# Kernel tuning notes

Hardware: AMD Instinct MI355X
Metric: run time of the kernel (lower is better)

The kernel has to match this reference:

```python
import jax, jax.numpy as jnp
import numpy as np

NEG_INF = -9e15


def setup_inputs() -> dict:
    key = jax.random.key(0)
    k1, k2, k3, k4, k5, k6 = jax.random.split(key, 6)
    B, N, F_IN, F_OUT = 16, 2048, 256, 128
    inputs = jax.random.normal(k1, (B, N, F_IN), dtype=jnp.float32)
    adj_matrix = jax.random.randint(k2, (B, N, N), 0, 2, dtype=jnp.int32)
    W = jax.random.normal(k3, (F_OUT, F_IN), dtype=jnp.float32) * (1.0 / np.sqrt(F_IN))
    b_W = jax.random.normal(k4, (F_OUT,), dtype=jnp.float32) * 0.02
    a = jax.random.normal(k5, (1, 2 * F_OUT), dtype=jnp.float32) * (1.0 / np.sqrt(2 * F_OUT))
    b_a = jax.random.normal(k6, (1,), dtype=jnp.float32) * 0.02
    return {"inputs": inputs, "adj_matrix": adj_matrix, "W": W, "b_W": b_W, "a": a, "b_a": b_a}


def reference(inputs, adj_matrix, W, b_W, a, b_a):
    # wh: [B, N, H]
    wh = jnp.einsum('bnf,hf->bnh', inputs, W) + b_W
    H = wh.shape[-1]
    # linear_self_W([wh_i, wh_j]) = a1.wh_i + a2.wh_j + b  (rank-1 linear over concat)
    a1 = a[0, :H]
    a2 = a[0, H:]
    src = jnp.einsum('bnh,h->bn', wh, a1)  # [B, N] contribution of row node i
    dst = jnp.einsum('bnh,h->bn', wh, a2)  # [B, N] contribution of col node j
    e = jax.nn.leaky_relu(src[:, :, None] + dst[:, None, :] + b_a[0], negative_slope=0.01)
    e = jnp.where(adj_matrix > 0, e, NEG_INF)
    att = jax.nn.softmax(e, axis=-1)  # dropout in eval mode = identity
    return jax.nn.elu(jnp.einsum('bij,bjh->bih', att, wh))
```

## Files before the change

kernel.cpp:

```cpp
#include <hip/hip_runtime.h>


#define BDIM 16
#define NDIM 2048
#define FIN 256
#define HDIM 128
#define LOG2E 1.4426950408889634f

typedef short short8 __attribute__((ext_vector_type(8)));
typedef float floatx4 __attribute__((ext_vector_type(4)));
typedef int intx4 __attribute__((ext_vector_type(4)));

__device__ __forceinline__ unsigned short f2bf(float x) {
    unsigned int u = __float_as_uint(x);
    unsigned int r = (u + 0x7fffu + ((u >> 16) & 1u)) >> 16;
    return (unsigned short)r;
}
__device__ __forceinline__ float bf2f(unsigned short s) {
    return __uint_as_float(((unsigned int)s) << 16);
}
__device__ __forceinline__ intx4 ldnt(const int* p) {
    return __builtin_nontemporal_load(reinterpret_cast<const intx4*>(p));
}

__global__ __launch_bounds__(256) void k_wh(const float* __restrict__ X,
                                            const float* __restrict__ W,
                                            const float* __restrict__ bW,
                                            const float* __restrict__ a,
                                            const float* __restrict__ ba_p,
                                            float* __restrict__ src,
                                            float* __restrict__ dst,
                                            unsigned short* __restrict__ whF) {
    __shared__ short lds[27648];
    short (*ah)[72] = (short(*)[72])lds;
    short (*al)[72] = (short(*)[72])(lds + 4608);
    short (*bh)[72] = (short(*)[72])(lds + 9216);
    short (*bl)[72] = (short(*)[72])(lds + 18432);
    short (*tb)[72] = (short(*)[72])lds;

    const int tid = threadIdx.x;
    const long row0 = (long)blockIdx.x * 64;
    const int w = tid >> 6, lane = tid & 63;
    const int lm = lane & 15, q = lane >> 4;
    const float ba0 = ba_p[0];

    float a1v[8], a2v[8], bwv[8];
    #pragma unroll
    for (int nt = 0; nt < 8; nt++) {
        a1v[nt] = a[nt * 16 + lm];
        a2v[nt] = a[HDIM + nt * 16 + lm];
        bwv[nt] = bW[nt * 16 + lm];
    }

    floatx4 acc[8];
    #pragma unroll
    for (int nt = 0; nt < 8; nt++) acc[nt] = (floatx4){0.f, 0.f, 0.f, 0.f};

    for (int k0 = 0; k0 < FIN; k0 += 64) {
        #pragma unroll
        for (int u = 0; u < 4; u++) {
            int idx = tid + u * 256;
            int r = idx >> 4, fc = (idx & 15) * 4;
            float4 v = *reinterpret_cast<const float4*>(X + (row0 + r) * FIN + k0 + fc);
            union { unsigned short s[4]; uint2 u2; } ph, pl;
            ph.s[0] = f2bf(v.x); pl.s[0] = f2bf(v.x - bf2f(ph.s[0]));
            ph.s[1] = f2bf(v.y); pl.s[1] = f2bf(v.y - bf2f(ph.s[1]));
            ph.s[2] = f2bf(v.z); pl.s[2] = f2bf(v.z - bf2f(ph.s[2]));
            ph.s[3] = f2bf(v.w); pl.s[3] = f2bf(v.w - bf2f(ph.s[3]));
            *reinterpret_cast<uint2*>(&ah[r][fc]) = ph.u2;
            *reinterpret_cast<uint2*>(&al[r][fc]) = pl.u2;
        }
        #pragma unroll
        for (int u = 0; u < 8; u++) {
            int idx = tid + u * 256;
            int hh = idx >> 4, fc = (idx & 15) * 4;
            float4 v = *reinterpret_cast<const float4*>(W + hh * FIN + k0 + fc);
            union { unsigned short s[4]; uint2 u2; } ph, pl;
            ph.s[0] = f2bf(v.x); pl.s[0] = f2bf(v.x - bf2f(ph.s[0]));
            ph.s[1] = f2bf(v.y); pl.s[1] = f2bf(v.y - bf2f(ph.s[1]));
            ph.s[2] = f2bf(v.z); pl.s[2] = f2bf(v.z - bf2f(ph.s[2]));
            ph.s[3] = f2bf(v.w); pl.s[3] = f2bf(v.w - bf2f(ph.s[3]));
            *reinterpret_cast<uint2*>(&bh[hh][fc]) = ph.u2;
            *reinterpret_cast<uint2*>(&bl[hh][fc]) = pl.u2;
        }
        __syncthreads();
        #pragma unroll
        for (int ks = 0; ks < 64; ks += 32) {
            short8 afh = *reinterpret_cast<const short8*>(&ah[w * 16 + lm][ks + q * 8]);
            short8 afl = *reinterpret_cast<const short8*>(&al[w * 16 + lm][ks + q * 8]);
            #pragma unroll
            for (int nt = 0; nt < 8; nt++) {
                short8 bfh = *reinterpret_cast<const short8*>(&bh[nt * 16 + lm][ks + q * 8]);
                short8 bfl = *reinterpret_cast<const short8*>(&bl[nt * 16 + lm][ks + q * 8]);
                acc[nt] = __builtin_amdgcn_mfma_f32_16x16x32_bf16(afh, bfh, acc[nt], 0, 0, 0);
                acc[nt] = __builtin_amdgcn_mfma_f32_16x16x32_bf16(afh, bfl, acc[nt], 0, 0, 0);
                acc[nt] = __builtin_amdgcn_mfma_f32_16x16x32_bf16(afl, bfh, acc[nt], 0, 0, 0);
            }
        }
        __syncthreads();
    }

    float s1[4] = {0.f, 0.f, 0.f, 0.f}, s2[4] = {0.f, 0.f, 0.f, 0.f};
    #pragma unroll
    for (int nt = 0; nt < 8; nt++) {
        #pragma unroll
        for (int r = 0; r < 4; r++) {
            float v = acc[nt][r] + bwv[nt];
            s1[r] += v * a1v[nt];
            s2[r] += v * a2v[nt];
            tb[nt * 16 + lm][w * 16 + q * 4 + r] = f2bf(v);
        }
    }
    #pragma unroll
    for (int r = 0; r < 4; r++) {
        #pragma unroll
        for (int o = 1; o < 16; o <<= 1) {
            s1[r] += __shfl_xor(s1[r], o);
            s2[r] += __shfl_xor(s2[r], o);
        }
    }
    if (lm == 0) {
        #pragma unroll
        for (int r = 0; r < 4; r++) {
            long row = row0 + w * 16 + q * 4 + r;
            src[row] = (s1[r] + ba0) * LOG2E;
            dst[row] = s2[r] * LOG2E;
        }
    }
    __syncthreads();
    const int b = (int)(row0 >> 11);
    const int jc0 = (int)((row0 & 2047) >> 5);
    const int f = tid >> 4;
    const int sub = tid & 15;
    const int jcrel = f >> 3, ht = f & 7;
    const size_t fbase = (((size_t)b * 64 + jc0 + jcrel) * 8 + ht) * 512;
    #pragma unroll
    for (int i = 0; i < 4; i++) {
        int l = sub * 4 + i;
        uint4 v = *reinterpret_cast<const uint4*>(&tb[ht * 16 + (l & 15)][jcrel * 32 + (l >> 4) * 8]);
        *reinterpret_cast<uint4*>(whF + fbase + l * 8) = v;
    }
}


#define BAR()                                                                  \
    do {                                                                       \
        asm volatile("s_waitcnt lgkmcnt(0)" ::: "memory");                     \
        __builtin_amdgcn_s_barrier();                                          \
    } while (0)

#define MD_PRE(PW1, BK, HI)                                                    \
    do {                                                                       \
        md[PW1][0] = maskB[BK][0 + (HI)][wrow];                                \
        md[PW1][1] = maskB[BK][2 + (HI)][wrow];                                \
        md[PW1][2] = maskB[BK][4 + (HI)][wrow];                                \
        md[PW1][3] = maskB[BK][6 + (HI)][wrow];                                \
    } while (0)

#define ADJ_ISSUE(GNEXT, H)                                                    \
    do {                                                                       \
        _Pragma("unroll")                                                      \
        for (int r = 0; r < 8; r++) {                                          \
            const int* ap = adj +                                              \
                (size_t)(rowbase + wave * 16 + (H) * 8 + r) * NDIM +           \
                (GNEXT) * 256 + lane * 4;                                      \
            av[r] = ldnt(ap);                                                  \
        }                                                                      \
    } while (0)

#define ADJ_BALLOT(GNEXT, H)                                                   \
    do {                                                                       \
        _Pragma("unroll")                                                      \
        for (int r = 0; r < 8; r++) {                                          \
            unsigned long long b0 = __ballot(av[r][0] != 0);                   \
            unsigned long long b1 = __ballot(av[r][1] != 0);                   \
            unsigned long long b2 = __ballot(av[r][2] != 0);                   \
            unsigned long long b3 = __ballot(av[r][3] != 0);                   \
            if (lane < 8) {                                                    \
                unsigned long long bb = (lane < 2) ? b0                        \
                                        : (lane < 4) ? b1                      \
                                        : (lane < 6) ? b2 : b3;                \
                unsigned wv = (lane & 1) ? (unsigned)(bb >> 32) : (unsigned)bb;\
                maskB[(GNEXT) & 1][lane][wave * 16 + (H) * 8 + r] = wv;        \
            }                                                                  \
        }                                                                      \
    } while (0)

#define CH(C)                                                                  \
    do {                                                                       \
        constexpr int PW = (C) & 1;                                            \
        const int T = g8 + (C);                                                \
        short8 s0, s1;                                                         \
        if (T < 63) {                 \
            const unsigned short* gp = gsrc + (size_t)(T + 1) * 4096;          \
            s0 = *reinterpret_cast<const short8*>(gp);                         \
            s1 = *reinterpret_cast<const short8*>(gp + 512);                   \
        }                                                                      \
        if ((C) == 0 && g8 < 56) ADJ_ISSUE((g8 >> 3) + 1, 0);                  \
        if ((C) == 3 && g8 < 56) {                                             \
            ADJ_BALLOT((g8 >> 3) + 1, 0);                                      \
            ADJ_ISSUE((g8 >> 3) + 1, 1);                                       \
        }                                                                      \
        if ((C) == 6 && g8 < 56) ADJ_BALLOT((g8 >> 3) + 1, 1);                 \
        if (T < 63) {                   \
            const float* dp = dstp + (T + 1) * 32;                             \
            d[PW ^ 1][0] = *reinterpret_cast<const floatx4*>(dp);              \
            d[PW ^ 1][1] = *reinterpret_cast<const floatx4*>(dp + 4);          \
            if ((C) < 7) {                                                     \
                MD_PRE(PW ^ 1, (g8 >> 3) & 1, (((C) + 1) & 4) ? 1 : 0);        \
            } else {                                                           \
                MD_PRE(PW ^ 1, ((g8 >> 3) + 1) & 1, 0);                        \
            }                                                                  \
        }                                                                      \
        const int base = 8 * ((C) & 3) + 2 * q;                                \
        short8 af;                                                             \
        _Pragma("unroll")                                                      \
        for (int j = 0; j < 8; j++) {                                          \
            float x = si + d[PW][j >> 2][j & 3];                               \
            x = fmaxf(x, 0.01f * x);               \
            float e2 = __builtin_amdgcn_exp2f(x);                              \
            unsigned bit = (md[PW][j & 3] >> (base + (j >> 2))) & 1u;          \
            float wgt = bit ? e2 : 0.f;                                        \
            lpart += wgt;                                                      \
            af[j] = (short)f2bf(wgt);                                          \
        }                                                                      \
        _Pragma("unroll")                                                      \
        for (int hj = 0; hj < 8; hj++) {                                       \
            short8 fb = *reinterpret_cast<const short8*>(                      \
                &whS[PW][hj * 512 + lane * 8]);                                \
            acc[hj] = __builtin_amdgcn_mfma_f32_16x16x32_bf16(af, fb,          \
                                                              acc[hj], 0, 0, 0); \
        }                                                                      \
        if (T < 63) {          \
            *reinterpret_cast<short8*>(&whS[PW ^ 1][pofs]) = s0;               \
            *reinterpret_cast<short8*>(&whS[PW ^ 1][pofs + 512]) = s1;         \
        }                                                                      \
        BAR();                                                                 \
    } while (0)

__global__ __launch_bounds__(256) void k_attn(const int* __restrict__ adj,
                                              const unsigned short* __restrict__ whF,
                                              const float* __restrict__ src,
                                              const float* __restrict__ dst,
                                              float* __restrict__ out) {
    __shared__ short whS[2][4096];
    __shared__ unsigned maskB[2][8][65];
    __shared__ float lred[64];
    __shared__ float linv_s[64];

    const int tid = threadIdx.x;
    const int bid = ((int)blockIdx.x & 7) * 64 + ((int)blockIdx.x >> 3);
    const int b = bid >> 5;
    const int i0 = (bid & 31) * 64;
    const int wave = tid >> 6, lane = tid & 63;
    const int lm = lane & 15, q = lane >> 4;
    const int wrow = wave * 16 + lm;
    const int rowbase = b * NDIM + i0;

    const float si = src[rowbase + wrow];
    const float* dstp = dst + b * NDIM + q * 8;
    const unsigned short* gsrc =
        whF + (size_t)b * 64 * 8 * 512 + wave * 1024 + lane * 8;
    const int pofs = wave * 1024 + lane * 8;

    floatx4 acc[8];
    #pragma unroll
    for (int hj = 0; hj < 8; hj++) acc[hj] = (floatx4){0.f, 0.f, 0.f, 0.f};
    float lpart = 0.f;

    unsigned md[2][4];
    floatx4 d[2][2];
    intx4 av[8];

    {
        short8 p0 = *reinterpret_cast<const short8*>(gsrc);
        short8 p1 = *reinterpret_cast<const short8*>(gsrc + 512);
        *reinterpret_cast<short8*>(&whS[0][pofs]) = p0;
        *reinterpret_cast<short8*>(&whS[0][pofs + 512]) = p1;
    }
    ADJ_ISSUE(0, 0);
    ADJ_BALLOT(0, 0);
    ADJ_ISSUE(0, 1);
    ADJ_BALLOT(0, 1);
    d[0][0] = *reinterpret_cast<const floatx4*>(dstp);
    d[0][1] = *reinterpret_cast<const floatx4*>(dstp + 4);
    __syncthreads();
    MD_PRE(0, 0, 0);

    for (int g8 = 0; g8 < 64; g8 += 8) {
        CH(0); CH(1); CH(2); CH(3);
        CH(4); CH(5); CH(6); CH(7);
    }

    lpart += __shfl_xor(lpart, 16);
    lpart += __shfl_xor(lpart, 32);
    if (q == 0) lred[wrow] = lpart;
    __syncthreads();
    if (tid < 64) {
        float l = lred[tid];
        linv_s[tid] = l > 0.f ? 1.f / l : 0.f;
    }
    __syncthreads();

    #pragma unroll
    for (int r = 0; r < 4; r++) {
        int il = wave * 16 + q * 4 + r;
        float li = linv_s[il];
        size_t obase = ((size_t)(rowbase + il)) * HDIM + lm;
        #pragma unroll
        for (int hj = 0; hj < 8; hj++) {
            float x = acc[hj][r] * li;
            x = x > 0.f ? x : (__expf(x) - 1.f);
            out[obase + hj * 16] = x;
        }
    }
}

extern "C" void kernel_launch(void* const* d_in, const int* in_sizes, int n_in,
                              void* d_out, int out_size, void* d_ws, size_t ws_size,
                              hipStream_t stream) {
    const float* X  = (const float*)d_in[0];
    const int* adj  = (const int*)d_in[1];
    const float* W  = (const float*)d_in[2];
    const float* bW = (const float*)d_in[3];
    const float* a  = (const float*)d_in[4];
    const float* ba = (const float*)d_in[5];
    float* out = (float*)d_out;

    float* srcv = (float*)d_ws;
    float* dstv = srcv + BDIM * NDIM;
    unsigned short* whF = (unsigned short*)(dstv + BDIM * NDIM);

    k_wh<<<BDIM * NDIM / 64, 256, 0, stream>>>(X, W, bW, a, ba, srcv, dstv, whF);
    k_attn<<<BDIM * (NDIM / 64), 256, 0, stream>>>(adj, whF, srcv, dstv, out);
}
```

Before: 410.6 us.

## Specialize waves: two stage wh tiles, two load adjacency masks; cache dst in LDS

Waves are split by role. Waves 0-1 now prefetch the full bf16 wh tile (four vectors each), and waves 2-3 issue and ballot all adjacency rows (16 rows per batch). The goal is to cut the per-wave count of mixed outstanding global loads and the scheduling contention between them. The dst vector for the batch is also loaded once into shared memory instead of from global every chunk. In exchange, register pressure rises in the adjacency waves (16 intx4 loads) and LDS use grows by 8KB, which may reduce occupancy, and load issue is no longer balanced across waves.

```diff
diff --git a/kernel.cpp b/kernel.cpp
--- a/kernel.cpp
+++ b/kernel.cpp
@@ -157,21 +157,21 @@
         md[PW1][3] = maskB[BK][6 + (HI)][wrow];                                \
     } while (0)
 
-#define ADJ_ISSUE(GNEXT, H)                                                    \
+#define ADJ_ISSUE(G, SUB)                                                      \
     do {                                                                       \
         _Pragma("unroll")                                                      \
-        for (int r = 0; r < 8; r++) {                                          \
+        for (int r = 0; r < 16; r++) {                                         \
             const int* ap = adj +                                              \
-                (size_t)(rowbase + wave * 16 + (H) * 8 + r) * NDIM +           \
-                (GNEXT) * 256 + lane * 4;                                      \
+                (size_t)(rowbase + aw32 + (SUB) * 16 + r) * NDIM +             \
+                (G) * 256 + lane * 4;                                          \
             av[r] = ldnt(ap);                                                  \
         }                                                                      \
     } while (0)
 
-#define ADJ_BALLOT(GNEXT, H)                                                   \
+#define ADJ_BALLOT(G, SUB)                                                     \
     do {                                                                       \
         _Pragma("unroll")                                                      \
-        for (int r = 0; r < 8; r++) {                                          \
+        for (int r = 0; r < 16; r++) {                                         \
             unsigned long long b0 = __ballot(av[r][0] != 0);                   \
             unsigned long long b1 = __ballot(av[r][1] != 0);                   \
             unsigned long long b2 = __ballot(av[r][2] != 0);                   \
@@ -181,7 +181,7 @@
                                         : (lane < 4) ? b1                      \
                                         : (lane < 6) ? b2 : b3;                \
                 unsigned wv = (lane & 1) ? (unsigned)(bb >> 32) : (unsigned)bb;\
-                maskB[(GNEXT) & 1][lane][wave * 16 + (H) * 8 + r] = wv;        \
+                maskB[(G) & 1][lane][aw32 + (SUB) * 16 + r] = wv;              \
             }                                                                  \
         }                                                                      \
     } while (0)
@@ -190,22 +190,28 @@
     do {                                                                       \
         constexpr int PW = (C) & 1;                                            \
         const int T = g8 + (C);                                                \
-        short8 s0, s1;                                                         \
-        if (T < 63) {                 \
-            const unsigned short* gp = gsrc + (size_t)(T + 1) * 4096;          \
-            s0 = *reinterpret_cast<const short8*>(gp);                         \
-            s1 = *reinterpret_cast<const short8*>(gp + 512);                   \
-        }                                                                      \
-        if ((C) == 0 && g8 < 56) ADJ_ISSUE((g8 >> 3) + 1, 0);                  \
-        if ((C) == 3 && g8 < 56) {                                             \
-            ADJ_BALLOT((g8 >> 3) + 1, 0);                                      \
-            ADJ_ISSUE((g8 >> 3) + 1, 1);                                       \
-        }                                                                      \
-        if ((C) == 6 && g8 < 56) ADJ_BALLOT((g8 >> 3) + 1, 1);                 \
-        if (T < 63) {                   \
-            const float* dp = dstp + (T + 1) * 32;                             \
-            d[PW ^ 1][0] = *reinterpret_cast<const floatx4*>(dp);              \
-            d[PW ^ 1][1] = *reinterpret_cast<const floatx4*>(dp + 4);          \
+        short8 s0, s1, s2, s3;                                                 \
+        if (wlow) {                                                            \
+            if (T < 63) {   \
+                const unsigned short* gp = gsrc + (size_t)(T + 1) * 4096;      \
+                s0 = *reinterpret_cast<const short8*>(gp);                     \
+                s1 = *reinterpret_cast<const short8*>(gp + 512);               \
+                s2 = *reinterpret_cast<const short8*>(gp + 1024);              \
+                s3 = *reinterpret_cast<const short8*>(gp + 1536);              \
+            }                                                                  \
+        } else {    \
+            if ((C) == 0 && g8 < 56) ADJ_ISSUE((g8 >> 3) + 1, 0);              \
+            if ((C) == 3 && g8 < 56) {                                         \
+                ADJ_BALLOT((g8 >> 3) + 1, 0);                                  \
+                ADJ_ISSUE((g8 >> 3) + 1, 1);                                   \
+            }                                                                  \
+            if ((C) == 6 && g8 < 56) ADJ_BALLOT((g8 >> 3) + 1, 1);             \
+        }                                                                      \
+        if (T < 63) {       \
+            d[PW ^ 1][0] =                                                     \
+                *reinterpret_cast<const floatx4*>(&dstS[(T + 1) * 32 + q8]);   \
+            d[PW ^ 1][1] =                                                     \
+                *reinterpret_cast<const floatx4*>(&dstS[(T + 1) * 32 + q8 + 4]); \
             if ((C) < 7) {                                                     \
                 MD_PRE(PW ^ 1, (g8 >> 3) & 1, (((C) + 1) & 4) ? 1 : 0);        \
             } else {                                                           \
@@ -231,9 +237,12 @@
             acc[hj] = __builtin_amdgcn_mfma_f32_16x16x32_bf16(af, fb,          \
                                                               acc[hj], 0, 0, 0); \
         }                                                                      \
-        if (T < 63) {          \
-            *reinterpret_cast<short8*>(&whS[PW ^ 1][pofs]) = s0;               \
-            *reinterpret_cast<short8*>(&whS[PW ^ 1][pofs + 512]) = s1;         \
+        if (wlow && T < 63) {       \
+            short* lp = &whS[PW ^ 1][pofs];                                    \
+            *reinterpret_cast<short8*>(lp) = s0;                               \
+            *reinterpret_cast<short8*>(lp + 512) = s1;                         \
+            *reinterpret_cast<short8*>(lp + 1024) = s2;                        \
+            *reinterpret_cast<short8*>(lp + 1536) = s3;                        \
         }                                                                      \
         BAR();                                                                 \
     } while (0)
@@ -245,6 +254,7 @@
                                               float* __restrict__ out) {
     __shared__ short whS[2][4096];
     __shared__ unsigned maskB[2][8][65];
+    __shared__ float dstS[2048];
     __shared__ float lred[64];
     __shared__ float linv_s[64];
 
@@ -253,15 +263,17 @@
     const int b = bid >> 5;
     const int i0 = (bid & 31) * 64;
     const int wave = tid >> 6, lane = tid & 63;
+    const bool wlow = wave < 2;
+    const int aw32 = (wave & 1) * 32;
     const int lm = lane & 15, q = lane >> 4;
+    const int q8 = q * 8;
     const int wrow = wave * 16 + lm;
     const int rowbase = b * NDIM + i0;
 
     const float si = src[rowbase + wrow];
-    const float* dstp = dst + b * NDIM + q * 8;
     const unsigned short* gsrc =
-        whF + (size_t)b * 64 * 8 * 512 + wave * 1024 + lane * 8;
-    const int pofs = wave * 1024 + lane * 8;
+        whF + (size_t)b * 262144 + wave * 2048 + lane * 8;
+    const int pofs = wave * 2048 + lane * 8;
 
     floatx4 acc[8];
     #pragma unroll
@@ -270,22 +282,35 @@
 
     unsigned md[2][4];
     floatx4 d[2][2];
-    intx4 av[8];
+    intx4 av[16];
 
     {
+        const float* dg = dst + b * NDIM;
+        *reinterpret_cast<float4*>(&dstS[tid * 8]) =
+            *reinterpret_cast<const float4*>(dg + tid * 8);
+        *reinterpret_cast<float4*>(&dstS[tid * 8 + 4]) =
+            *reinterpret_cast<const float4*>(dg + tid * 8 + 4);
+    }
+    if (wlow) {
         short8 p0 = *reinterpret_cast<const short8*>(gsrc);
         short8 p1 = *reinterpret_cast<const short8*>(gsrc + 512);
-        *reinterpret_cast<short8*>(&whS[0][pofs]) = p0;
-        *reinterpret_cast<short8*>(&whS[0][pofs + 512]) = p1;
-    }
-    ADJ_ISSUE(0, 0);
-    ADJ_BALLOT(0, 0);
-    ADJ_ISSUE(0, 1);
-    ADJ_BALLOT(0, 1);
-    d[0][0] = *reinterpret_cast<const floatx4*>(dstp);
-    d[0][1] = *reinterpret_cast<const floatx4*>(dstp + 4);
+        short8 p2 = *reinterpret_cast<const short8*>(gsrc + 1024);
+        short8 p3 = *reinterpret_cast<const short8*>(gsrc + 1536);
+        short* lp = &whS[0][pofs];
+        *reinterpret_cast<short8*>(lp) = p0;
+        *reinterpret_cast<short8*>(lp + 512) = p1;
+        *reinterpret_cast<short8*>(lp + 1024) = p2;
+        *reinterpret_cast<short8*>(lp + 1536) = p3;
+    } else {
+        ADJ_ISSUE(0, 0);
+        ADJ_BALLOT(0, 0);
+        ADJ_ISSUE(0, 1);
+        ADJ_BALLOT(0, 1);
+    }
     __syncthreads();
     MD_PRE(0, 0, 0);
+    d[0][0] = *reinterpret_cast<const floatx4*>(&dstS[q8]);
+    d[0][1] = *reinterpret_cast<const floatx4*>(&dstS[q8 + 4]);
 
     for (int g8 = 0; g8 < 64; g8 += 8) {
         CH(0); CH(1); CH(2); CH(3);
```

Measured after the change: 457.4 us. 11.4% more time.
